# Performance work log

Hardware: AMD Instinct MI355X
Metric: run time of the kernel (lower is better)

## Reference

```python
import jax, jax.numpy as jnp
import numpy as np

B, S, E, H, D, R = 2, 2048, 1024, 16, 64, 16


def setup_inputs() -> dict:
    key = jax.random.key(0)
    ks = jax.random.split(key, 9)
    s = lambda k, shape, fan: jax.random.normal(k, shape, dtype=jnp.float32) / np.sqrt(fan)
    return {
        "x": jax.random.normal(ks[0], (B, S, E), dtype=jnp.float32),
        "Wq": s(ks[1], (H, E, D), E),
        "bq": jnp.zeros((H, D), jnp.float32),
        "Wk": s(ks[2], (H, E, D), E),
        "bk": jnp.zeros((H, D), jnp.float32),
        "Wvd": s(ks[3], (H, E, R), E),
        "bvd": jnp.zeros((H, R), jnp.float32),
        "Wvu": s(ks[4], (H, R, D), R),
        "bvu": jnp.zeros((H, D), jnp.float32),
    }


def reference(x, Wq, bq, Wk, bk, Wvd, bvd, Wvu, bvu):
    b, s, e = x.shape
    # per-head projections, vectorized over heads h
    q = jnp.einsum('bse,hed->bhsd', x, Wq) + bq[None, :, None, :]
    k = jnp.einsum('bse,hed->bhsd', x, Wk) + bk[None, :, None, :]
    # NOTE: original scales by sqrt(embedding_dimension), not head dim
    scores = jnp.einsum('bhsd,bhtd->bhst', q, k) / jnp.sqrt(jnp.float32(e))
    # original mask: masked_fill where key_idx < query_idx (anti-causal)
    qi = jnp.arange(s)[:, None]
    ki = jnp.arange(s)[None, :]
    scores = jnp.where(ki < qi, -jnp.inf, scores)
    att = jax.nn.softmax(scores, axis=-1)  # dropout p=0 (eval)
    # low-rank value: up(down(x))
    vd = jnp.einsum('bse,her->bhsr', x, Wvd) + bvd[None, :, None, :]
    v = jnp.einsum('bhsr,hrd->bhsd', vd, Wvu) + bvu[None, :, None, :]
    out = jnp.einsum('bhst,bhtd->bhsd', att, v)
    # concat heads along last dim (head order = stack order)
    return out.transpose(0, 2, 1, 3).reshape(b, s, -1)
```

## Files before the change

kernel.cpp:

```cpp
#include <hip/hip_runtime.h>
#include <stdint.h>

#define B_ 2
#define S_ 2048
#define E_ 1024
#define H_ 16
#define D_ 64
#define R_ 16

typedef short s16x8 __attribute__((ext_vector_type(8)));
typedef float f32x4 __attribute__((ext_vector_type(4)));

#define K1_ 0.045084220027780106f
#define K0_ -28.853900817779268f

__device__ __forceinline__ unsigned short f2bf(float f) {
  union { float f; unsigned u; } v; v.f = f;
  return (unsigned short)((v.u + 0x8000u) >> 16);
}

__device__ __forceinline__ void load_lds16(const void* g, void* l) {
  __builtin_amdgcn_global_load_lds(
      (__attribute__((address_space(1))) void*)(g),
      (__attribute__((address_space(3))) void*)(l), 16, 0, 0);
}

__global__ void k_prep(const float* __restrict__ x,
                       const float* __restrict__ Wq, const float* __restrict__ Wk,
                       const float* __restrict__ Wvd, const float* __restrict__ Wvu,
                       const float* __restrict__ bq, const float* __restrict__ bk,
                       const float* __restrict__ bvd, const float* __restrict__ bvu,
                       unsigned short* __restrict__ xb, unsigned short* __restrict__ Wt,
                       float* __restrict__ ball) {
  __shared__ float T[64][65];
  const int blk = blockIdx.x;
  const int t = threadIdx.x;
  if (blk < 4096) {
    int i = (blk * 256 + t) * 4;
    float4 v = *(const float4*)(x + i);
    ushort4 o;
    o.x = f2bf(v.x); o.y = f2bf(v.y); o.z = f2bf(v.z); o.w = f2bf(v.w);
    *(ushort4*)(xb + i) = o;
  } else if (blk < 4608) {
    const int bb = blk - 4096;
    const int which = bb >> 8;
    const int h = (bb >> 4) & 15;
    const int et = bb & 15;
    const float scl = which ? 1.f : K1_;
    const float* src = (which ? Wk : Wq) + (h * E_ + et * 64) * D_;
#pragma unroll
    for (int pr = 0; pr < 4; ++pr) {
      const int row = pr * 16 + (t >> 4);
      const int col = (t & 15) * 4;
      float4 v = *(const float4*)(src + row * 64 + col);
      T[row][col] = v.x; T[row][col + 1] = v.y; T[row][col + 2] = v.z; T[row][col + 3] = v.w;
    }
    __syncthreads();
#pragma unroll
    for (int pr = 0; pr < 4; ++pr) {
      const int d = pr * 16 + (t >> 4);
      const int ec = (t & 15) * 4;
      ushort4 o;
      o.x = f2bf(T[ec][d] * scl); o.y = f2bf(T[ec + 1][d] * scl);
      o.z = f2bf(T[ec + 2][d] * scl); o.w = f2bf(T[ec + 3][d] * scl);
      *(ushort4*)(Wt + ((which << 10) + h * 64 + d) * 1024 + et * 64 + ec) = o;
    }
  } else if (blk < 8704) {
    const int idx = (blk - 4608) * 256 + t;
    const int row = idx >> 10;
    const int e = idx & 1023;
    const int h = row >> 6, d = row & 63;
    const float4* wd4 = (const float4*)(Wvd + (h << 14) + e * 16);
    const float* wu = Wvu + h * R_ * D_ + d;
    float acc = 0.f;
#pragma unroll
    for (int r4 = 0; r4 < 4; ++r4) {
      float4 a = wd4[r4];
      acc += a.x * wu[(r4 * 4 + 0) * 64];
      acc += a.y * wu[(r4 * 4 + 1) * 64];
      acc += a.z * wu[(r4 * 4 + 2) * 64];
      acc += a.w * wu[(r4 * 4 + 3) * 64];
    }
    Wt[(2048 + row) * 1024 + e] = f2bf(acc);
  } else {
    int n = (blk - 8704) * 256 + t;
    int which = n >> 10;
    int hd = n & 1023;
    int h = hd >> 6, d = hd & 63;
    float v;
    if (which == 0) v = bq[hd] * K1_;
    else if (which == 1) v = bk[hd];
    else {
      v = bvu[hd];
#pragma unroll
      for (int r = 0; r < R_; ++r) v += bvd[h * R_ + r] * Wvu[(h * R_ + r) * D_ + d];
    }
    ball[n] = v;
  }
}


__global__ __launch_bounds__(256, 2) void k_gemm_qkv(
    const unsigned short* __restrict__ X, const unsigned short* __restrict__ Wt,
    const float* __restrict__ ball,
    unsigned short* __restrict__ Qb, unsigned short* __restrict__ Kb,
    unsigned short* __restrict__ Vb) {
  __shared__ unsigned short As[128 * 32];
  __shared__ unsigned short Bs[128 * 32];
  const int tid = threadIdx.x;
  const int lane = tid & 63, wave = tid >> 6;
  const int quad = lane >> 4, l16 = lane & 15;
  const int mBase = blockIdx.y * 128, nBase = blockIdx.x * 128;
  const int wm = (wave & 1) * 64, wn = (wave >> 1) * 64;
  const int lrow = lane >> 2, lcol = (lane & 3) * 8;

  f32x4 acc[4][4];
#pragma unroll
  for (int mi = 0; mi < 4; ++mi)
#pragma unroll
    for (int ni = 0; ni < 4; ++ni) acc[mi][ni] = (f32x4){0.f, 0.f, 0.f, 0.f};

  for (int k0 = 0; k0 < E_; k0 += 32) {
#pragma unroll
    for (int i = 0; i < 2; ++i) {
      const int r0 = __builtin_amdgcn_readfirstlane((wave + i * 4) * 16);
      load_lds16(X + (mBase + r0 + lrow) * E_ + k0 + lcol, &As[r0 * 32]);
      load_lds16(Wt + (nBase + r0 + lrow) * E_ + k0 + lcol, &Bs[r0 * 32]);
    }
    __syncthreads();
    s16x8 af[4], bfr[4];
#pragma unroll
    for (int mi = 0; mi < 4; ++mi)
      af[mi] = *(const s16x8*)&As[(wm + mi * 16 + l16) * 32 + quad * 8];
#pragma unroll
    for (int ni = 0; ni < 4; ++ni)
      bfr[ni] = *(const s16x8*)&Bs[(wn + ni * 16 + l16) * 32 + quad * 8];
#pragma unroll
    for (int mi = 0; mi < 4; ++mi)
#pragma unroll
      for (int ni = 0; ni < 4; ++ni)
        acc[mi][ni] = __builtin_amdgcn_mfma_f32_16x16x32_bf16(af[mi], bfr[ni], acc[mi][ni], 0, 0, 0);
    __syncthreads();
  }

  const int which = nBase >> 10;
#pragma unroll
  for (int ni = 0; ni < 4; ++ni) {
    const int n = nBase + wn + ni * 16 + l16;
    const int nh = n & 1023;
    const int h = nh >> 6, d = nh & 63;
    const float bias = ball[n];
#pragma unroll
    for (int mi = 0; mi < 4; ++mi) {
      const int m0 = mBase + wm + mi * 16 + quad * 4;
      const int b = m0 >> 11;
      const int s = m0 & 2047;
      const int bh = b * H_ + h;
      if (which == 2) {
        ushort4 pk;
        pk.x = f2bf(acc[mi][ni][0] + bias);
        pk.y = f2bf(acc[mi][ni][1] + bias);
        pk.z = f2bf(acc[mi][ni][2] + bias);
        pk.w = f2bf(acc[mi][ni][3] + bias);
        *(ushort4*)(Vb + (bh * D_ + d) * S_ + s) = pk;
      } else {
        unsigned short* dst = (which == 0 ? Qb : Kb) + (bh * S_ + s) * D_ + d;
#pragma unroll
        for (int r = 0; r < 4; ++r) dst[r * D_] = f2bf(acc[mi][ni][r] + bias);
      }
    }
  }
}


__global__ __launch_bounds__(256, 4) void k_attn(
    const unsigned short* __restrict__ Qb, const unsigned short* __restrict__ Kb,
    const unsigned short* __restrict__ Vb, float* __restrict__ out) {
  __shared__ unsigned short Ks[2][2 * 64 * 32];
  __shared__ unsigned short Vs[2][2 * 64 * 32];
  __shared__ unsigned short Ps[4][16][40];
  const int tid = threadIdx.x;
  const int lane = tid & 63, wave = tid >> 6;
  const int quad = lane >> 4, l16 = lane & 15;
  const int chunk = blockIdx.x >> 8;
  const int j = blockIdx.x & 255;
  int qt = j >> 3;
  if (chunk & 1) qt = 31 - qt;
  const int bh = (j & 7) + 8 * chunk;
  const int q0 = qt * 64;
  const int lrow = lane >> 2, lcol = (lane & 3) * 8;
  const int r0 = __builtin_amdgcn_readfirstlane(wave * 16);
  const f32x4 kvec = {K0_, K0_, K0_, K0_};

  s16x8 qf[2];
  {
    const unsigned short* qp = Qb + (bh * S_ + q0 + wave * 16 + l16) * D_ + quad * 8;
    qf[0] = *(const s16x8*)qp;
    qf[1] = *(const s16x8*)(qp + 32);
  }
  f32x4 o[4];
#pragma unroll
  for (int dc = 0; dc < 4; ++dc) o[dc] = (f32x4){0.f, 0.f, 0.f, 0.f};
  float l_acc[4] = {0.f, 0.f, 0.f, 0.f};

#define DMA_KV(kt_, b_)                                                          \
  {                                                                              \
    _Pragma("unroll")                                                            \
    for (int hdc = 0; hdc < 2; ++hdc) {                                          \
      load_lds16(Kb + (bh * S_ + (kt_) * 64 + r0 + lrow) * D_ + hdc * 32 + lcol, \
                 &Ks[b_][hdc * 2048 + r0 * 32]);                                 \
      load_lds16(Vb + (bh * D_ + r0 + lrow) * S_ + (kt_) * 64 + hdc * 32 + lcol, \
                 &Vs[b_][hdc * 2048 + r0 * 32]);                                 \
    }                                                                            \
  }

  DMA_KV(qt, 0);

  int buf = 0;
  for (int kt = qt; kt < S_ / 64; ++kt) {
    __syncthreads();
    if (kt + 1 < S_ / 64) DMA_KV(kt + 1, buf ^ 1);

    const bool diag = (kt == qt);
#pragma unroll
    for (int kc = 0; kc < 2; ++kc) {
#pragma unroll
      for (int tcc = 0; tcc < 2; ++tcc) {
        const int tc = kc * 2 + tcc;
        f32x4 a = __builtin_amdgcn_mfma_f32_16x16x32_bf16(
            qf[0], *(const s16x8*)&Ks[buf][(tc * 16 + l16) * 32 + quad * 8], kvec, 0, 0, 0);
        f32x4 sc = __builtin_amdgcn_mfma_f32_16x16x32_bf16(
            qf[1], *(const s16x8*)&Ks[buf][2048 + (tc * 16 + l16) * 32 + quad * 8], a, 0, 0, 0);
        if (diag) {
#pragma unroll
          for (int r = 0; r < 4; ++r) {
            const int t = tc * 16 + l16;
            const int q = wave * 16 + quad * 4 + r;
            if (t < q) sc[r] = -200.f;
          }
        }
#pragma unroll
        for (int r = 0; r < 4; ++r) {
          float p = exp2f(sc[r]);
          l_acc[r] += p;
          Ps[wave][quad * 4 + r][tcc * 16 + l16] =
              (unsigned short)(__float_as_uint(p) >> 16);
        }
      }
      s16x8 pf = *(const s16x8*)&Ps[wave][l16][quad * 8];
#pragma unroll
      for (int dc = 0; dc < 4; ++dc) {
        s16x8 vb = *(const s16x8*)&Vs[buf][kc * 2048 + (dc * 16 + l16) * 32 + quad * 8];
        o[dc] = __builtin_amdgcn_mfma_f32_16x16x32_bf16(pf, vb, o[dc], 0, 0, 0);
      }
    }
    buf ^= 1;
  }
#undef DMA_KV

#pragma unroll
  for (int off = 1; off < 16; off <<= 1)
#pragma unroll
    for (int r = 0; r < 4; ++r) l_acc[r] += __shfl_xor(l_acc[r], off);
  float rinv[4];
#pragma unroll
  for (int r = 0; r < 4; ++r) rinv[r] = 1.f / l_acc[r];

  const int b = bh >> 4, h = bh & 15;
#pragma unroll
  for (int dc = 0; dc < 4; ++dc)
#pragma unroll
    for (int r = 0; r < 4; ++r) {
      const int s = q0 + wave * 16 + quad * 4 + r;
      out[(b * S_ + s) * (H_ * D_) + h * D_ + dc * 16 + l16] = o[dc][r] * rinv[r];
    }
}


extern "C" void kernel_launch(void* const* d_in, const int* in_sizes, int n_in,
                              void* d_out, int out_size, void* d_ws, size_t ws_size,
                              hipStream_t stream) {
  const float* x   = (const float*)d_in[0];
  const float* Wq  = (const float*)d_in[1];
  const float* bq  = (const float*)d_in[2];
  const float* Wk  = (const float*)d_in[3];
  const float* bk  = (const float*)d_in[4];
  const float* Wvd = (const float*)d_in[5];
  const float* bvd = (const float*)d_in[6];
  const float* Wvu = (const float*)d_in[7];
  const float* bvu = (const float*)d_in[8];
  float* out = (float*)d_out;

  char* ws = (char*)d_ws;
  unsigned short* xb   = (unsigned short*)(ws);
  unsigned short* Wt   = (unsigned short*)(ws + (8u << 20));
  float*          ball = (float*)(ws + (14u << 20));
  unsigned short* Qb   = (unsigned short*)(ws + (15u << 20));
  unsigned short* Kb   = (unsigned short*)(ws + (23u << 20));
  unsigned short* Vb   = (unsigned short*)(ws + (31u << 20));

  k_prep<<<8716, 256, 0, stream>>>(x, Wq, Wk, Wvd, Wvu, bq, bk, bvd, bvu, xb, Wt, ball);
  k_gemm_qkv<<<dim3(3072 / 128, 4096 / 128), 256, 0, stream>>>(xb, Wt, ball, Qb, Kb, Vb);
  k_attn<<<1024, 256, 0, stream>>>(Qb, Kb, Vb, out);
}
```

Baseline: 170.2 us.

## Compute transposed scores and pass P to PV MFMA via register shuffles

Swaps the QK^T MFMA operands so each lane holds scores for one query row across four keys. The exponentiated probabilities are then packed to bf16 with v_cvt_pk_bf16 and rearranged into the PV A-operand layout with cross-lane shuffles, instead of a round trip through an LDS P buffer. This removes the per-wave LDS writes and reads and shrinks the row-sum reduction, at the cost of extra shuffles and selects. The bf16 conversion also changes from truncation to the instruction's rounding.

Result: no change. 173.0 us (+1.6%).

```diff
diff --git a/kernel.cpp b/kernel.cpp
--- a/kernel.cpp
+++ b/kernel.cpp
@@ -17,6 +17,12 @@
 __device__ __forceinline__ unsigned short f2bf(float f) {
   union { float f; unsigned u; } v; v.f = f;
   return (unsigned short)((v.u + 0x8000u) >> 16);
+}
+
+__device__ __forceinline__ unsigned cvt_pk_bf16(float a, float b) {
+  unsigned r;
+  asm("v_cvt_pk_bf16_f32 %0, %1, %2" : "=v"(r) : "v"(a), "v"(b));
+  return r;
 }
 
 __device__ __forceinline__ void load_lds16(const void* g, void* l) {
@@ -172,13 +178,11 @@
   }
 }
 
-
 __global__ __launch_bounds__(256, 4) void k_attn(
     const unsigned short* __restrict__ Qb, const unsigned short* __restrict__ Kb,
     const unsigned short* __restrict__ Vb, float* __restrict__ out) {
   __shared__ unsigned short Ks[2][2 * 64 * 32];
   __shared__ unsigned short Vs[2][2 * 64 * 32];
-  __shared__ unsigned short Ps[4][16][40];
   const int tid = threadIdx.x;
   const int lane = tid & 63, wave = tid >> 6;
   const int quad = lane >> 4, l16 = lane & 15;
@@ -201,7 +205,8 @@
   f32x4 o[4];
 #pragma unroll
   for (int dc = 0; dc < 4; ++dc) o[dc] = (f32x4){0.f, 0.f, 0.f, 0.f};
-  float l_acc[4] = {0.f, 0.f, 0.f, 0.f};
+  float l_acc = 0.f;
+  const int qloc = wave * 16 + l16;
 
 #define DMA_KV(kt_, b_)                                                          \
   {                                                                              \
@@ -222,49 +227,61 @@
     if (kt + 1 < S_ / 64) DMA_KV(kt + 1, buf ^ 1);
 
     const bool diag = (kt == qt);
+    const bool hi32 = (lane >= 32);
+    const bool oddq = (lane & 16) != 0;
 #pragma unroll
     for (int kc = 0; kc < 2; ++kc) {
+      unsigned c0, c1, c2, c3;
 #pragma unroll
       for (int tcc = 0; tcc < 2; ++tcc) {
         const int tc = kc * 2 + tcc;
         f32x4 a = __builtin_amdgcn_mfma_f32_16x16x32_bf16(
-            qf[0], *(const s16x8*)&Ks[buf][(tc * 16 + l16) * 32 + quad * 8], kvec, 0, 0, 0);
+            *(const s16x8*)&Ks[buf][(tc * 16 + l16) * 32 + quad * 8], qf[0], kvec, 0, 0, 0);
         f32x4 sc = __builtin_amdgcn_mfma_f32_16x16x32_bf16(
-            qf[1], *(const s16x8*)&Ks[buf][2048 + (tc * 16 + l16) * 32 + quad * 8], a, 0, 0, 0);
+            *(const s16x8*)&Ks[buf][2048 + (tc * 16 + l16) * 32 + quad * 8], qf[1], a, 0, 0, 0);
         if (diag) {
-#pragma unroll
-          for (int r = 0; r < 4; ++r) {
-            const int t = tc * 16 + l16;
-            const int q = wave * 16 + quad * 4 + r;
-            if (t < q) sc[r] = -200.f;
-          }
+          const int tb = tc * 16 + quad * 4;
+#pragma unroll
+          for (int r = 0; r < 4; ++r)
+            if (tb + r < qloc) sc[r] = -200.f;
         }
-#pragma unroll
-        for (int r = 0; r < 4; ++r) {
-          float p = exp2f(sc[r]);
-          l_acc[r] += p;
-          Ps[wave][quad * 4 + r][tcc * 16 + l16] =
-              (unsigned short)(__float_as_uint(p) >> 16);
-        }
+        const float p0 = exp2f(sc[0]);
+        const float p1 = exp2f(sc[1]);
+        const float p2 = exp2f(sc[2]);
+        const float p3 = exp2f(sc[3]);
+        l_acc += (p0 + p1) + (p2 + p3);
+        const unsigned lo = cvt_pk_bf16(p0, p1);
+        const unsigned hi = cvt_pk_bf16(p2, p3);
+        if (tcc == 0) { c0 = lo; c1 = hi; } else { c2 = lo; c3 = hi; }
       }
-      s16x8 pf = *(const s16x8*)&Ps[wave][l16][quad * 8];
+      unsigned a0, a1, a2, a3;
+      { unsigned s = __shfl_xor(c0, 32), t = __shfl_xor(c2, 32);
+        a0 = hi32 ? t : c0; a2 = hi32 ? c2 : s; }
+      { unsigned s = __shfl_xor(c1, 32), t = __shfl_xor(c3, 32);
+        a1 = hi32 ? t : c1; a3 = hi32 ? c3 : s; }
+      unsigned u0, u1, u2, u3;
+      { unsigned s = __shfl_xor(a0, 16), t = __shfl_xor(a2, 16);
+        u0 = oddq ? t : a0; u2 = oddq ? a2 : s; }
+      { unsigned s = __shfl_xor(a1, 16), t = __shfl_xor(a3, 16);
+        u1 = oddq ? t : a1; u3 = oddq ? a3 : s; }
+      union { s16x8 v; unsigned u[4]; } pa;
+      pa.u[0] = u0; pa.u[1] = u1; pa.u[2] = u2; pa.u[3] = u3;
 #pragma unroll
       for (int dc = 0; dc < 4; ++dc) {
         s16x8 vb = *(const s16x8*)&Vs[buf][kc * 2048 + (dc * 16 + l16) * 32 + quad * 8];
-        o[dc] = __builtin_amdgcn_mfma_f32_16x16x32_bf16(pf, vb, o[dc], 0, 0, 0);
+        o[dc] = __builtin_amdgcn_mfma_f32_16x16x32_bf16(pa.v, vb, o[dc], 0, 0, 0);
       }
     }
     buf ^= 1;
   }
 #undef DMA_KV
 
-#pragma unroll
-  for (int off = 1; off < 16; off <<= 1)
-#pragma unroll
-    for (int r = 0; r < 4; ++r) l_acc[r] += __shfl_xor(l_acc[r], off);
-  float rinv[4];
-#pragma unroll
-  for (int r = 0; r < 4; ++r) rinv[r] = 1.f / l_acc[r];
+  l_acc += __shfl_xor(l_acc, 16);
+  l_acc += __shfl_xor(l_acc, 32);
+  const float rinv = 1.f / l_acc;
+  float rv[4];
+#pragma unroll
+  for (int r = 0; r < 4; ++r) rv[r] = __shfl(rinv, quad * 4 + r);
 
   const int b = bh >> 4, h = bh & 15;
 #pragma unroll
@@ -272,7 +289,7 @@
 #pragma unroll
     for (int r = 0; r < 4; ++r) {
       const int s = q0 + wave * 16 + quad * 4 + r;
-      out[(b * S_ + s) * (H_ * D_) + h * D_ + dc * 16 + l16] = o[dc][r] * rinv[r];
+      out[(b * S_ + s) * (H_ * D_) + h * D_ + dc * 16 + l16] = o[dc][r] * rv[r];
     }
 }
 
```

## Process two query groups per attention block and swizzle K/V LDS layout

Applied to the files above, without the earlier changes.

Each attention block now covers 128 query rows split into two 64-row groups, so every K/V tile loaded into LDS and every K fragment read feeds twice as many MFMAs. Alongside this, the K/V DMA destination and read addresses are XOR-swizzled to cut LDS bank conflicts. The grid shrinks to 512 blocks with launch bounds lowered to 2 blocks per CU, so register pressure and occupancy trade against the reuse gain. The diagonal masking now spans two key tiles per block.

Result: slower. 180.3 us (+6.0%).

```diff
diff --git a/kernel.cpp b/kernel.cpp
--- a/kernel.cpp
+++ b/kernel.cpp
@@ -172,86 +172,106 @@
   }
 }
 
-
-__global__ __launch_bounds__(256, 4) void k_attn(
+__global__ __launch_bounds__(256, 2) void k_attn(
     const unsigned short* __restrict__ Qb, const unsigned short* __restrict__ Kb,
     const unsigned short* __restrict__ Vb, float* __restrict__ out) {
   __shared__ unsigned short Ks[2][2 * 64 * 32];
   __shared__ unsigned short Vs[2][2 * 64 * 32];
-  __shared__ unsigned short Ps[4][16][40];
+  __shared__ unsigned short Ps[4][32][40];
   const int tid = threadIdx.x;
   const int lane = tid & 63, wave = tid >> 6;
   const int quad = lane >> 4, l16 = lane & 15;
   const int chunk = blockIdx.x >> 8;
   const int j = blockIdx.x & 255;
-  int qt = j >> 3;
-  if (chunk & 1) qt = 31 - qt;
-  const int bh = (j & 7) + 8 * chunk;
-  const int q0 = qt * 64;
-  const int lrow = lane >> 2, lcol = (lane & 3) * 8;
+  int qt = j >> 5;
+  if (chunk) qt = 15 - qt;
+  const int bh = j & 31;
+  const int q0 = qt * 128;
   const int r0 = __builtin_amdgcn_readfirstlane(wave * 16);
   const f32x4 kvec = {K0_, K0_, K0_, K0_};
 
-  s16x8 qf[2];
-  {
-    const unsigned short* qp = Qb + (bh * S_ + q0 + wave * 16 + l16) * D_ + quad * 8;
-    qf[0] = *(const s16x8*)qp;
-    qf[1] = *(const s16x8*)(qp + 32);
-  }
-  f32x4 o[4];
-#pragma unroll
-  for (int dc = 0; dc < 4; ++dc) o[dc] = (f32x4){0.f, 0.f, 0.f, 0.f};
-  float l_acc[4] = {0.f, 0.f, 0.f, 0.f};
-
-#define DMA_KV(kt_, b_)                                                          \
-  {                                                                              \
-    _Pragma("unroll")                                                            \
-    for (int hdc = 0; hdc < 2; ++hdc) {                                          \
-      load_lds16(Kb + (bh * S_ + (kt_) * 64 + r0 + lrow) * D_ + hdc * 32 + lcol, \
-                 &Ks[b_][hdc * 2048 + r0 * 32]);                                 \
-      load_lds16(Vb + (bh * D_ + r0 + lrow) * S_ + (kt_) * 64 + hdc * 32 + lcol, \
-                 &Vs[b_][hdc * 2048 + r0 * 32]);                                 \
-    }                                                                            \
-  }
-
-  DMA_KV(qt, 0);
+  const int lrow = lane >> 2;
+  const int q3w  = ((lrow & 1) << 2) | (lane & 3);
+  const int q3e  = q3w ^ ((lrow >> 1) & 7);
+  const int sr16 = (lrow & ~1) | (q3e >> 2);
+  const int sc   = (q3e & 3) * 8;
+
+  const int rbase = (l16 >> 1) * 64 + ((((l16 & 1) << 2) | quad) ^ ((l16 >> 1) & 7)) * 8;
+
+  s16x8 qf[2][2];
+#pragma unroll
+  for (int g = 0; g < 2; ++g) {
+    const unsigned short* qp = Qb + (bh * S_ + q0 + g * 64 + wave * 16 + l16) * D_ + quad * 8;
+    qf[g][0] = *(const s16x8*)qp;
+    qf[g][1] = *(const s16x8*)(qp + 32);
+  }
+  f32x4 o[2][4];
+  float l_acc[2][4];
+#pragma unroll
+  for (int g = 0; g < 2; ++g)
+#pragma unroll
+    for (int dc = 0; dc < 4; ++dc) {
+      o[g][dc] = (f32x4){0.f, 0.f, 0.f, 0.f};
+      l_acc[g][dc] = 0.f;
+    }
+
+#define DMA_KV(kt_, b_)                                                           \
+  {                                                                               \
+    _Pragma("unroll")                                                             \
+    for (int hdc = 0; hdc < 2; ++hdc) {                                           \
+      load_lds16(Kb + (bh * S_ + (kt_) * 64 + r0 + sr16) * D_ + hdc * 32 + sc,    \
+                 &Ks[b_][hdc * 2048 + r0 * 32]);                                  \
+      load_lds16(Vb + (bh * D_ + r0 + sr16) * S_ + (kt_) * 64 + hdc * 32 + sc,    \
+                 &Vs[b_][hdc * 2048 + r0 * 32]);                                  \
+    }                                                                             \
+  }
+
+  DMA_KV(2 * qt, 0);
 
   int buf = 0;
-  for (int kt = qt; kt < S_ / 64; ++kt) {
+  for (int kt = 2 * qt; kt < S_ / 64; ++kt) {
     __syncthreads();
     if (kt + 1 < S_ / 64) DMA_KV(kt + 1, buf ^ 1);
 
-    const bool diag = (kt == qt);
+    const bool diag = (kt < 2 * qt + 2);
 #pragma unroll
     for (int kc = 0; kc < 2; ++kc) {
-#pragma unroll
-      for (int tcc = 0; tcc < 2; ++tcc) {
-        const int tc = kc * 2 + tcc;
-        f32x4 a = __builtin_amdgcn_mfma_f32_16x16x32_bf16(
-            qf[0], *(const s16x8*)&Ks[buf][(tc * 16 + l16) * 32 + quad * 8], kvec, 0, 0, 0);
-        f32x4 sc = __builtin_amdgcn_mfma_f32_16x16x32_bf16(
-            qf[1], *(const s16x8*)&Ks[buf][2048 + (tc * 16 + l16) * 32 + quad * 8], a, 0, 0, 0);
-        if (diag) {
+      s16x8 kf[2][2];
+#pragma unroll
+      for (int tcc = 0; tcc < 2; ++tcc)
+#pragma unroll
+        for (int hdc = 0; hdc < 2; ++hdc)
+          kf[tcc][hdc] = *(const s16x8*)&Ks[buf][hdc * 2048 + (kc * 2 + tcc) * 512 + rbase];
+#pragma unroll
+      for (int g = 0; g < 2; ++g) {
+#pragma unroll
+        for (int tcc = 0; tcc < 2; ++tcc) {
+          const int tc = kc * 2 + tcc;
+          f32x4 a = __builtin_amdgcn_mfma_f32_16x16x32_bf16(qf[g][0], kf[tcc][0], kvec, 0, 0, 0);
+          f32x4 sc4 = __builtin_amdgcn_mfma_f32_16x16x32_bf16(qf[g][1], kf[tcc][1], a, 0, 0, 0);
+          if (diag) {
+            const int t = kt * 64 + tc * 16 + l16;
+            const int q = q0 + g * 64 + wave * 16 + quad * 4;
+#pragma unroll
+            for (int r = 0; r < 4; ++r)
+              if (t < q + r) sc4[r] = -200.f;
+          }
 #pragma unroll
           for (int r = 0; r < 4; ++r) {
-            const int t = tc * 16 + l16;
-            const int q = wave * 16 + quad * 4 + r;
-            if (t < q) sc[r] = -200.f;
+            float p = exp2f(sc4[r]);
+            l_acc[g][r] += p;
+            Ps[wave][g * 16 + quad * 4 + r][tcc * 16 + l16] =
+                (unsigned short)(__float_as_uint(p) >> 16);
           }
         }
-#pragma unroll
-        for (int r = 0; r < 4; ++r) {
-          float p = exp2f(sc[r]);
-          l_acc[r] += p;
-          Ps[wave][quad * 4 + r][tcc * 16 + l16] =
-              (unsigned short)(__float_as_uint(p) >> 16);
-        }
       }
-      s16x8 pf = *(const s16x8*)&Ps[wave][l16][quad * 8];
+      s16x8 pf0 = *(const s16x8*)&Ps[wave][l16][quad * 8];
+      s16x8 pf1 = *(const s16x8*)&Ps[wave][16 + l16][quad * 8];
 #pragma unroll
       for (int dc = 0; dc < 4; ++dc) {
-        s16x8 vb = *(const s16x8*)&Vs[buf][kc * 2048 + (dc * 16 + l16) * 32 + quad * 8];
-        o[dc] = __builtin_amdgcn_mfma_f32_16x16x32_bf16(pf, vb, o[dc], 0, 0, 0);
+        s16x8 vb = *(const s16x8*)&Vs[buf][kc * 2048 + dc * 512 + rbase];
+        o[0][dc] = __builtin_amdgcn_mfma_f32_16x16x32_bf16(pf0, vb, o[0][dc], 0, 0, 0);
+        o[1][dc] = __builtin_amdgcn_mfma_f32_16x16x32_bf16(pf1, vb, o[1][dc], 0, 0, 0);
       }
     }
     buf ^= 1;
@@ -261,19 +281,25 @@
 #pragma unroll
   for (int off = 1; off < 16; off <<= 1)
 #pragma unroll
-    for (int r = 0; r < 4; ++r) l_acc[r] += __shfl_xor(l_acc[r], off);
-  float rinv[4];
-#pragma unroll
-  for (int r = 0; r < 4; ++r) rinv[r] = 1.f / l_acc[r];
+    for (int g = 0; g < 2; ++g)
+#pragma unroll
+      for (int r = 0; r < 4; ++r) l_acc[g][r] += __shfl_xor(l_acc[g][r], off);
+  float rinv[2][4];
+#pragma unroll
+  for (int g = 0; g < 2; ++g)
+#pragma unroll
+    for (int r = 0; r < 4; ++r) rinv[g][r] = 1.f / l_acc[g][r];
 
   const int b = bh >> 4, h = bh & 15;
 #pragma unroll
-  for (int dc = 0; dc < 4; ++dc)
-#pragma unroll
-    for (int r = 0; r < 4; ++r) {
-      const int s = q0 + wave * 16 + quad * 4 + r;
-      out[(b * S_ + s) * (H_ * D_) + h * D_ + dc * 16 + l16] = o[dc][r] * rinv[r];
-    }
+  for (int g = 0; g < 2; ++g)
+#pragma unroll
+    for (int dc = 0; dc < 4; ++dc)
+#pragma unroll
+      for (int r = 0; r < 4; ++r) {
+        const int s = q0 + g * 64 + wave * 16 + quad * 4 + r;
+        out[(b * S_ + s) * (H_ * D_) + h * D_ + dc * 16 + l16] = o[g][dc][r] * rinv[g][r];
+      }
 }
 
 
@@ -301,5 +327,5 @@
 
   k_prep<<<8716, 256, 0, stream>>>(x, Wq, Wk, Wvd, Wvu, bq, bk, bvd, bvu, xb, Wt, ball);
   k_gemm_qkv<<<dim3(3072 / 128, 4096 / 128), 256, 0, stream>>>(xb, Wt, ball, Qb, Kb, Vb);
-  k_attn<<<1024, 256, 0, stream>>>(Qb, Kb, Vb, out);
-}
+  k_attn<<<512, 256, 0, stream>>>(Qb, Kb, Vb, out);
+}
```

## Triple-buffer K/V tiles with vmcnt waits and XOR-swizzled LDS layout

Applied to the files above, without the earlier changes.

Moves the attention kernel's K/V staging from double to triple buffering. It prefetches two tiles ahead and replaces __syncthreads with an explicit s_waitcnt vmcnt plus s_barrier, so loads stay in flight across iterations. It also XOR-swizzles the global-to-LDS row/column mapping to cut LDS bank conflicts on the MFMA operand reads. In exchange, LDS use rises and the occupancy hint drops from 4 to 3 blocks per CU, and the hand-written vmcnt count depends on exactly four loads being issued per tile.

New measurement: 193.1 us. 1.13x slower.

```diff
diff --git a/kernel.cpp b/kernel.cpp
--- a/kernel.cpp
+++ b/kernel.cpp
@@ -172,12 +172,11 @@
   }
 }
 
-
-__global__ __launch_bounds__(256, 4) void k_attn(
+__global__ __launch_bounds__(256, 3) void k_attn(
     const unsigned short* __restrict__ Qb, const unsigned short* __restrict__ Kb,
     const unsigned short* __restrict__ Vb, float* __restrict__ out) {
-  __shared__ unsigned short Ks[2][2 * 64 * 32];
-  __shared__ unsigned short Vs[2][2 * 64 * 32];
+  __shared__ unsigned short Ks[3][2 * 64 * 32];
+  __shared__ unsigned short Vs[3][2 * 64 * 32];
   __shared__ unsigned short Ps[4][16][40];
   const int tid = threadIdx.x;
   const int lane = tid & 63, wave = tid >> 6;
@@ -188,9 +187,15 @@
   if (chunk & 1) qt = 31 - qt;
   const int bh = (j & 7) + 8 * chunk;
   const int q0 = qt * 64;
-  const int lrow = lane >> 2, lcol = (lane & 3) * 8;
   const int r0 = __builtin_amdgcn_readfirstlane(wave * 16);
   const f32x4 kvec = {K0_, K0_, K0_, K0_};
+
+  const int lrow = lane >> 2;
+  const int q3w  = ((lrow & 1) << 2) | (lane & 3);
+  const int q3e  = q3w ^ ((lrow >> 1) & 7);
+  const int sr16 = (lrow & ~1) | (q3e >> 2);
+  const int sc   = (q3e & 3) * 8;
+  const int rbase = (l16 >> 1) * 64 + ((((l16 & 1) << 2) | quad) ^ ((l16 >> 1) & 7)) * 8;
 
   s16x8 qf[2];
   {
@@ -203,23 +208,29 @@
   for (int dc = 0; dc < 4; ++dc) o[dc] = (f32x4){0.f, 0.f, 0.f, 0.f};
   float l_acc[4] = {0.f, 0.f, 0.f, 0.f};
 
-#define DMA_KV(kt_, b_)                                                          \
-  {                                                                              \
-    _Pragma("unroll")                                                            \
-    for (int hdc = 0; hdc < 2; ++hdc) {                                          \
-      load_lds16(Kb + (bh * S_ + (kt_) * 64 + r0 + lrow) * D_ + hdc * 32 + lcol, \
-                 &Ks[b_][hdc * 2048 + r0 * 32]);                                 \
-      load_lds16(Vb + (bh * D_ + r0 + lrow) * S_ + (kt_) * 64 + hdc * 32 + lcol, \
-                 &Vs[b_][hdc * 2048 + r0 * 32]);                                 \
-    }                                                                            \
+#define DMA_KV(kt_, b_)                                                           \
+  {                                                                               \
+    _Pragma("unroll")                                                             \
+    for (int hdc = 0; hdc < 2; ++hdc) {                                           \
+      load_lds16(Kb + (bh * S_ + (kt_) * 64 + r0 + sr16) * D_ + hdc * 32 + sc,    \
+                 &Ks[b_][hdc * 2048 + r0 * 32]);                                  \
+      load_lds16(Vb + (bh * D_ + r0 + sr16) * S_ + (kt_) * 64 + hdc * 32 + sc,    \
+                 &Vs[b_][hdc * 2048 + r0 * 32]);                                  \
+    }                                                                             \
   }
 
   DMA_KV(qt, 0);
-
-  int buf = 0;
+  if (qt + 1 < S_ / 64) DMA_KV(qt + 1, 1);
+
+  int cur = 0;
   for (int kt = qt; kt < S_ / 64; ++kt) {
-    __syncthreads();
-    if (kt + 1 < S_ / 64) DMA_KV(kt + 1, buf ^ 1);
+    if (kt + 1 < S_ / 64) asm volatile("s_waitcnt vmcnt(4)" ::: "memory");
+    else                  asm volatile("s_waitcnt vmcnt(0)" ::: "memory");
+    asm volatile("s_barrier" ::: "memory");
+    if (kt + 2 < S_ / 64) {
+      int b2 = cur + 2; if (b2 >= 3) b2 -= 3;
+      DMA_KV(kt + 2, b2);
+    }
 
     const bool diag = (kt == qt);
 #pragma unroll
@@ -228,20 +239,20 @@
       for (int tcc = 0; tcc < 2; ++tcc) {
         const int tc = kc * 2 + tcc;
         f32x4 a = __builtin_amdgcn_mfma_f32_16x16x32_bf16(
-            qf[0], *(const s16x8*)&Ks[buf][(tc * 16 + l16) * 32 + quad * 8], kvec, 0, 0, 0);
-        f32x4 sc = __builtin_amdgcn_mfma_f32_16x16x32_bf16(
-            qf[1], *(const s16x8*)&Ks[buf][2048 + (tc * 16 + l16) * 32 + quad * 8], a, 0, 0, 0);
+            qf[0], *(const s16x8*)&Ks[cur][tc * 512 + rbase], kvec, 0, 0, 0);
+        f32x4 sc4 = __builtin_amdgcn_mfma_f32_16x16x32_bf16(
+            qf[1], *(const s16x8*)&Ks[cur][2048 + tc * 512 + rbase], a, 0, 0, 0);
         if (diag) {
 #pragma unroll
           for (int r = 0; r < 4; ++r) {
             const int t = tc * 16 + l16;
             const int q = wave * 16 + quad * 4 + r;
-            if (t < q) sc[r] = -200.f;
+            if (t < q) sc4[r] = -200.f;
           }
         }
 #pragma unroll
         for (int r = 0; r < 4; ++r) {
-          float p = exp2f(sc[r]);
+          float p = exp2f(sc4[r]);
           l_acc[r] += p;
           Ps[wave][quad * 4 + r][tcc * 16 + l16] =
               (unsigned short)(__float_as_uint(p) >> 16);
@@ -250,11 +261,11 @@
       s16x8 pf = *(const s16x8*)&Ps[wave][l16][quad * 8];
 #pragma unroll
       for (int dc = 0; dc < 4; ++dc) {
-        s16x8 vb = *(const s16x8*)&Vs[buf][kc * 2048 + (dc * 16 + l16) * 32 + quad * 8];
+        s16x8 vb = *(const s16x8*)&Vs[cur][kc * 2048 + dc * 512 + rbase];
         o[dc] = __builtin_amdgcn_mfma_f32_16x16x32_bf16(pf, vb, o[dc], 0, 0, 0);
       }
     }
-    buf ^= 1;
+    ++cur; if (cur == 3) cur = 0;
   }
 #undef DMA_KV
 
```
